# Performance work log

Hardware: AMD Instinct MI355X
Metric: run time of the kernel (lower is better)

The kernel has to match this reference:

```python
import jax, jax.numpy as jnp
import numpy as np

B, SEQ, VOCAB, DIM, DEPTH, HEADS, DH, M, FF, LABELS = 4, 2048, 4096, 768, 6, 12, 64, 256, 3072, 2
INNER = HEADS * DH
EPS_K = 1e-4  # FAVOR+ kernel eps
EPS_LN = 1e-5


def setup_inputs() -> dict:
    key = jax.random.key(0)
    ks = jax.random.split(key, 16)
    g = lambda k, shape: (jax.random.normal(k, shape, jnp.float32) * 0.02)
    return {
        "x": jax.random.randint(ks[0], (B, SEQ), 0, VOCAB),
        "token_emb": g(ks[1], (VOCAB, DIM)),
        "pos_emb": g(ks[2], (SEQ, DIM)),
        "ln1_g": jnp.ones((DEPTH, DIM)), "ln1_b": jnp.zeros((DEPTH, DIM)),
        "Wq": g(ks[3], (DEPTH, DIM, INNER)),
        "Wk": g(ks[4], (DEPTH, DIM, INNER)),
        "Wv": g(ks[5], (DEPTH, DIM, INNER)),
        "Wo": g(ks[6], (DEPTH, INNER, DIM)), "bo": jnp.zeros((DEPTH, DIM)),
        "proj": jax.random.normal(ks[7], (DEPTH, M, DH), jnp.float32),  # FAVOR+ random projections (buffer)
        "ln2_g": jnp.ones((DEPTH, DIM)), "ln2_b": jnp.zeros((DEPTH, DIM)),
        "W1": g(ks[8], (DEPTH, DIM, FF)), "b1": jnp.zeros((DEPTH, FF)),
        "W2": g(ks[9], (DEPTH, FF, DIM)), "b2": jnp.zeros((DEPTH, DIM)),
        "lnf_g": jnp.ones((DIM,)), "lnf_b": jnp.zeros((DIM,)),
        "Wp": g(ks[10], (DIM, DIM)), "bp": jnp.zeros((DIM,)),
        "Wc": g(ks[11], (DIM, LABELS)), "bc": jnp.zeros((LABELS,)),
    }


def layernorm(x, g, b):
    mu = jnp.mean(x, -1, keepdims=True)
    var = jnp.mean(jnp.square(x - mu), -1, keepdims=True)
    return (x - mu) * jax.lax.rsqrt(var + EPS_LN) * g + b


def softmax_kernel(x, proj, is_query):
    # x: [b,h,n,d]  proj: [m,d]   (FAVOR+ positive softmax features)
    d = x.shape[-1]
    m = proj.shape[0]
    dn = d ** -0.25            # data normalizer 1/sqrt(sqrt(d))
    ratio = m ** -0.5
    xd = jnp.einsum('bhnd,md->bhnm', x * dn, proj)
    diag = 0.5 * jnp.sum(jnp.square(x), -1, keepdims=True) * (dn * dn)  # [b,h,n,1]
    if is_query:
        stab = jnp.max(xd, axis=-1, keepdims=True)
    else:
        stab = jnp.max(xd, axis=(-2, -1), keepdims=True)
    return ratio * (jnp.exp(xd - diag - stab) + EPS_K)


def favor_attention(y, Wq, Wk, Wv, Wo, bo, proj):
    b, n, _ = y.shape
    split = lambda t: t.reshape(b, n, HEADS, DH).transpose(0, 2, 1, 3)  # -> bhnd
    q, k, v = split(y @ Wq), split(y @ Wk), split(y @ Wv)
    qp = softmax_kernel(q, proj, True)    # [b,h,n,m]
    kp = softmax_kernel(k, proj, False)   # [b,h,n,m]
    k_sum = jnp.sum(kp, axis=2)                                  # [b,h,m]
    d_inv = 1.0 / jnp.einsum('bhnm,bhm->bhn', qp, k_sum)
    ctx = jnp.einsum('bhnm,bhnd->bhmd', kp, v)                   # [b,h,m,d]
    out = jnp.einsum('bhmd,bhnm,bhn->bhnd', ctx, qp, d_inv)
    out = out.transpose(0, 2, 1, 3).reshape(b, n, INNER)
    return out @ Wo + bo


def reference(x, token_emb, pos_emb, ln1_g, ln1_b, Wq, Wk, Wv, Wo, bo, proj,
              ln2_g, ln2_b, W1, b1, W2, b2, lnf_g, lnf_b, Wp, bp, Wc, bc):
    n = x.shape[1]
    h = token_emb[x] + pos_emb[None, :n]
    for l in range(DEPTH):
        h = h + favor_attention(layernorm(h, ln1_g[l], ln1_b[l]),
                                Wq[l], Wk[l], Wv[l], Wo[l], bo[l], proj[l])
        y = layernorm(h, ln2_g[l], ln2_b[l])
        h = h + (jax.nn.gelu(y @ W1[l] + b1[l], approximate=False) @ W2[l] + b2[l])
    h = layernorm(h, lnf_g, lnf_b)
    pooled = jnp.tanh(h[:, 0] @ Wp + bp)   # BertPooler on first token
    return pooled @ Wc + bc                 # [B, LABELS]
```

## Files before the change

### kernel.cpp

```cpp
#include <hip/hip_runtime.h>
#include <hip/hip_bf16.h>
#include <math.h>

#define B_ 4
#define SEQ_ 2048
#define DIM_ 768
#define DEPTH_ 6
#define HEADS_ 12
#define DH_ 64
#define MF_ 256
#define FF_ 3072
#define ROWS_ 8192
#define BH_ 48
#define QKVW_ 2304
#define DN_ 0.3535533905932738f
#define RATIO_ 0.0625f
#define EPSK_ 1e-4f
#define EPSLN_ 1e-5f

typedef unsigned short u16;
typedef unsigned int   u32;
typedef __bf16 bf16x8 __attribute__((ext_vector_type(8)));
typedef u16    u16x8  __attribute__((ext_vector_type(8)));
typedef float  f32x4  __attribute__((ext_vector_type(4)));

__device__ inline u16 f2bf(float x){
  u32 u = __builtin_bit_cast(u32, x);
  return (u16)((u + 0x7FFFu + ((u>>16)&1u)) >> 16);
}
__device__ inline float bf2f(u16 v){ return __builtin_bit_cast(float, (u32)v<<16); }

__device__ inline void gload16(const u16* g, u16* lds){
  __builtin_amdgcn_global_load_lds(
    (const __attribute__((address_space(1))) u32*)(const void*)g,
    (__attribute__((address_space(3))) u32*)(void*)lds, 16, 0, 0);
}

__global__ void embed_kernel(const int* __restrict__ x, const float4* __restrict__ tok,
                             const float4* __restrict__ pos, float4* __restrict__ h){
  const int C4 = DIM_/4;
  long total = (long)ROWS_*C4;
  for (long i = (long)blockIdx.x*blockDim.x + threadIdx.x; i < total;
       i += (long)gridDim.x*blockDim.x){
    int row = (int)(i / C4); int c = (int)(i - (long)row*C4);
    int n = row & (SEQ_-1);
    float4 a = tok[(long)x[row]*C4 + c];
    float4 p = pos[(long)n*C4 + c];
    float4 o; o.x=a.x+p.x; o.y=a.y+p.y; o.z=a.z+p.z; o.w=a.w+p.w;
    h[i] = o;
  }
}

__global__ __launch_bounds__(256) void ln_kernel(const float* __restrict__ X,
                          const float* __restrict__ g, const float* __restrict__ bta,
                          u16* __restrict__ Y){
  int row = blockIdx.x; int t = threadIdx.x;
  const float* xr = X + (long)row*DIM_;
  float v0 = xr[t], v1 = xr[t+256], v2 = xr[t+512];
  float s = v0+v1+v2;
  float ss = v0*v0+v1*v1+v2*v2;
  int lane = t&63, wid = t>>6;
  #pragma unroll
  for (int off=32; off; off>>=1){ s += __shfl_xor(s,off); ss += __shfl_xor(ss,off); }
  __shared__ float red[8];
  if (lane==0){ red[wid]=s; red[4+wid]=ss; }
  __syncthreads();
  s  = red[0]+red[1]+red[2]+red[3];
  ss = red[4]+red[5]+red[6]+red[7];
  float mu  = s*(1.0f/DIM_);
  float var = ss*(1.0f/DIM_) - mu*mu;
  float rs  = rsqrtf(var + EPSLN_);
  u16* yr = Y + (long)row*DIM_;
  yr[t]     = f2bf((v0-mu)*rs*g[t]     + bta[t]);
  yr[t+256] = f2bf((v1-mu)*rs*g[t+256] + bta[t+256]);
  yr[t+512] = f2bf((v2-mu)*rs*g[t+512] + bta[t+512]);
}

__global__ __launch_bounds__(256) void tconv_kernel(const float* __restrict__ W,
        u16* __restrict__ WT, int K, int N){
  __shared__ float tile[32][33];
  int n0 = blockIdx.x*32, k0 = blockIdx.y*32;
  int tx = threadIdx.x & 31, ty = threadIdx.x >> 5;
  #pragma unroll
  for (int i=0;i<32;i+=8) tile[ty+i][tx] = W[(long)(k0+ty+i)*N + n0+tx];
  __syncthreads();
  #pragma unroll
  for (int i=0;i<32;i+=8) WT[(long)(n0+ty+i)*K + k0+tx] = f2bf(tile[tx][ty+i]);
}

__global__ __launch_bounds__(256) void tconv4_kernel(const float* __restrict__ Wq,
        const float* __restrict__ Wk, const float* __restrict__ Wv,
        const float* __restrict__ Wo, u16* __restrict__ dst){
  __shared__ float tile[32][33];
  int z = blockIdx.z;
  const float* W = (z==0)?Wq:(z==1)?Wk:(z==2)?Wv:Wo;
  u16* WT = dst + (long)z*589824;
  int n0 = blockIdx.x*32, k0 = blockIdx.y*32;
  int tx = threadIdx.x & 31, ty = threadIdx.x >> 5;
  #pragma unroll
  for (int i=0;i<32;i+=8) tile[ty+i][tx] = W[(long)(k0+ty+i)*768 + n0+tx];
  __syncthreads();
  #pragma unroll
  for (int i=0;i<32;i+=8) WT[(long)(n0+ty+i)*768 + k0+tx] = f2bf(tile[tx][ty+i]);
}

template<int FM, int FN, int WM, int WN, int ACT, int CMODE, int BATCH>
__global__ __launch_bounds__(256) void mgemm(const u16* __restrict__ A,
     const u16* __restrict__ BT, const float* __restrict__ bias,
     void* __restrict__ Cv, const float* __restrict__ scale,
     int M, int N, int K, int ldC){
  (void)M;
  constexpr int BM = WM*FM*16, BN = WN*FN*16;
  constexpr int ACH = BM/16, BCH = BN/16;
  __shared__ u16 As[BM*64];
  __shared__ u16 Bs[BN*64];
  int tid = threadIdx.x; int w = tid>>6, l = tid&63;
  int bx, by;
  if (BATCH){ bx = blockIdx.x; by = blockIdx.y; }
  else {
    int bid = blockIdx.y*gridDim.x + blockIdx.x;
    int cpx = (gridDim.x*gridDim.y) >> 3;
    int swz = (bid & 7)*cpx + (bid >> 3);
    bx = swz % gridDim.x; by = swz / gridDim.x;
  }
  int m0 = by*BM, n0 = bx*BN;
  long coff = 0, srow0 = 0;
  if (BATCH){
    int z = blockIdx.z;
    A  += (long)z*2048*K;
    BT += (long)z*(long)N*K;
    coff  = (long)(z/HEADS_)*SEQ_*(long)ldC + (long)(z%HEADS_)*64;
    srow0 = (long)z*SEQ_;
  }
  f32x4 acc[FM][FN];
  #pragma unroll
  for (int i=0;i<FM;i++)
    #pragma unroll
    for (int j=0;j<FN;j++) acc[i][j] = (f32x4){0.f,0.f,0.f,0.f};

  const int row_l = l>>2, cq_l = l&3;
  const int wm = w / WN, wn = w % WN;
  const int kq = l>>4, rl15 = l&15;

  for (int k0=0; k0<K; k0+=64){
    __syncthreads();
    for (int c = w; c < 2*ACH; c += 4){
      int rc = c>>1, ks = c&1;
      int r = rc*16 + row_l;
      int gq = cq_l ^ ((r>>1)&3);
      gload16(A + (long)(m0+r)*K + k0 + ks*32 + gq*8, As + c*512);
    }
    for (int c = w; c < 2*BCH; c += 4){
      int rc = c>>1, ks = c&1;
      int r = rc*16 + row_l;
      int gq = cq_l ^ ((r>>1)&3);
      gload16(BT + (long)(n0+r)*K + k0 + ks*32 + gq*8, Bs + c*512);
    }
    __syncthreads();
    #pragma unroll
    for (int ks=0; ks<2; ks++){
      bf16x8 af[FM], bfr[FN];
      #pragma unroll
      for (int mi=0; mi<FM; mi++){
        int rr = (wm*FM + mi)*16 + rl15;
        int g = kq ^ ((rr>>1)&3);
        af[mi] = *(const bf16x8*)(As + ((rr>>4)*2 + ks)*512 + (rr&15)*32 + g*8);
      }
      #pragma unroll
      for (int ni=0; ni<FN; ni++){
        int rr = (wn*FN + ni)*16 + rl15;
        int g = kq ^ ((rr>>1)&3);
        bfr[ni] = *(const bf16x8*)(Bs + ((rr>>4)*2 + ks)*512 + (rr&15)*32 + g*8);
      }
      #pragma unroll
      for (int mi=0; mi<FM; mi++)
        #pragma unroll
        for (int ni=0; ni<FN; ni++)
          acc[mi][ni] = __builtin_amdgcn_mfma_f32_16x16x32_bf16(af[mi], bfr[ni], acc[mi][ni], 0, 0, 0);
    }
  }

  int cc = l&15, rq = l>>4;
  #pragma unroll
  for (int mi=0; mi<FM; mi++){
    #pragma unroll
    for (int ni=0; ni<FN; ni++){
      int gcol = n0 + (wn*FN+ni)*16 + cc;
      float bv = bias ? bias[gcol] : 0.f;
      #pragma unroll
      for (int r4=0; r4<4; r4++){
        int grow = m0 + (wm*FM+mi)*16 + rq*4 + r4;
        float v = acc[mi][ni][r4] + bv;
        if (ACT) v = 0.5f*v*(1.0f + erff(v*0.70710678118654752f));
        if (CMODE==1){
          float* C = (float*)Cv;
          C[(long)grow*ldC + gcol] += v;
        } else if (CMODE==2){
          v *= scale[srow0 + grow];
          ((u16*)Cv)[coff + (long)grow*ldC + gcol] = f2bf(v);
        } else {
          ((u16*)Cv)[(long)grow*ldC + gcol] = f2bf(v);
        }
      }
    }
  }
}

__global__ void projcvt_kernel(const float* __restrict__ p, u16* __restrict__ hi,
                               u16* __restrict__ lo){
  int i = blockIdx.x*256 + threadIdx.x;
  float v = p[i];
  u16 h = f2bf(v);
  hi[i] = h;
  lo[i] = f2bf(v - bf2f(h));
}

__global__ __launch_bounds__(256) void diag2_kernel(const u16* __restrict__ qkvp,
        float* __restrict__ diagq, float* __restrict__ diagk){
  int chunk = blockIdx.x, z = blockIdx.y, which = blockIdx.z, t = threadIdx.x;
  const u16* X = qkvp + (which ? 768 : 0);
  float* outp = which ? diagk : diagq;
  int n = chunk*256 + t;
  const u16* r = X + ((long)(z/HEADS_)*SEQ_ + n)*QKVW_ + (z%HEADS_)*DH_;
  float s = 0.f;
  #pragma unroll
  for (int q=0;q<8;q++){
    u16x8 v = *(const u16x8*)(r + q*8);
    #pragma unroll
    for (int j=0;j<8;j++){ float f = bf2f(v[j]); s += f*f; }
  }
  outp[(long)z*SEQ_ + n] = 0.5f*DN_*DN_*s;
}

template<int MODE>
__global__ __launch_bounds__(256) void featgemm(const u16* __restrict__ X,
     const u16* __restrict__ PB, const float* __restrict__ diag,
     const float* __restrict__ stab, u16* __restrict__ kp,
     float* __restrict__ fmaxp){
  __shared__ u16 As[128*32];
  __shared__ u16 Bs[128*32];
  __shared__ float wred[4];
  int tid = threadIdx.x; int w = tid>>6, l = tid&63;
  int n0 = blockIdx.x*128, m0 = blockIdx.y*128;
  int z = blockIdx.z;
  const u16* A = X + (long)(z/HEADS_)*SEQ_*QKVW_ + (z%HEADS_)*DH_;
  f32x4 acc[4][4];
  #pragma unroll
  for (int i=0;i<4;i++)
    #pragma unroll
    for (int j=0;j<4;j++) acc[i][j] = (f32x4){0.f,0.f,0.f,0.f};
  const int row_l = l>>2, cq_l = l&3;
  const int wm = w>>1, wn = w&1;
  const int kq = l>>4, rl15 = l&15;

  for (int k0=0; k0<64; k0+=32){
    __syncthreads();
    for (int c = w; c < 8; c += 4){
      int r = c*16 + row_l;
      int gq = cq_l ^ ((r>>1)&3);
      gload16(A + (long)(m0+r)*QKVW_ + k0 + gq*8, As + c*512);
    }
    for (int c = w; c < 8; c += 4){
      int r = c*16 + row_l;
      int gq = cq_l ^ ((r>>1)&3);
      gload16(PB + (long)(n0+r)*64 + k0 + gq*8, Bs + c*512);
    }
    __syncthreads();
    bf16x8 af[4], bfr[4];
    #pragma unroll
    for (int mi=0; mi<4; mi++){
      int rr = (wm*4 + mi)*16 + rl15;
      int g = kq ^ ((rr>>1)&3);
      af[mi] = *(const bf16x8*)(As + rr*32 + g*8);
    }
    #pragma unroll
    for (int ni=0; ni<4; ni++){
      int rr = (wn*4 + ni)*16 + rl15;
      int g = kq ^ ((rr>>1)&3);
      bfr[ni] = *(const bf16x8*)(Bs + rr*32 + g*8);
    }
    #pragma unroll
    for (int mi=0; mi<4; mi++)
      #pragma unroll
      for (int ni=0; ni<4; ni++)
        acc[mi][ni] = __builtin_amdgcn_mfma_f32_16x16x32_bf16(af[mi], bfr[ni], acc[mi][ni], 0, 0, 0);
  }

  if (MODE==0){
    float bm = -1e30f;
    #pragma unroll
    for (int mi=0;mi<4;mi++)
      #pragma unroll
      for (int ni=0;ni<4;ni++)
        #pragma unroll
        for (int r4=0;r4<4;r4++) bm = fmaxf(bm, acc[mi][ni][r4]);
    bm *= DN_;
    #pragma unroll
    for (int off=32; off; off>>=1) bm = fmaxf(bm, __shfl_xor(bm,off));
    if (l==0) wred[w] = bm;
    __syncthreads();
    if (tid==0)
      fmaxp[z*32 + blockIdx.y*2 + blockIdx.x] =
        fmaxf(fmaxf(wred[0],wred[1]),fmaxf(wred[2],wred[3]));
  } else {
    __shared__ float ksred[128][8];
    float st = stab[z];
    int cc = l&15, rq = l>>4;
    #pragma unroll
    for (int ni=0; ni<4; ni++){
      int gcol = n0 + (wn*4+ni)*16 + cc;
      float cs = 0.f;
      #pragma unroll
      for (int mi=0; mi<4; mi++){
        #pragma unroll
        for (int r4=0; r4<4; r4++){
          int grow = m0 + (wm*4+mi)*16 + rq*4 + r4;
          float v = acc[mi][ni][r4]*DN_;
          float e = RATIO_*(expf(v - diag[(long)z*SEQ_ + grow] - st) + EPSK_);
          u16 eb = f2bf(e);
          kp[((long)z*SEQ_ + grow)*MF_ + gcol] = eb;
          cs += bf2f(eb);
        }
      }
      ksred[(wn*4+ni)*16 + cc][wm*4 + rq] = cs;
    }
    __syncthreads();
    if (tid < 128){
      float s = 0.f;
      #pragma unroll
      for (int q=0;q<8;q++) s += ksred[tid][q];
      fmaxp[((long)z*16 + blockIdx.y)*MF_ + n0 + tid] = s;
    }
  }
}

__global__ void fmax_reduce(const float* __restrict__ fmaxp, float* __restrict__ stab){
  int z = blockIdx.x, t = threadIdx.x;
  float m = (t<32) ? fmaxp[z*32+t] : -1e30f;
  #pragma unroll
  for (int off=32; off; off>>=1) m = fmaxf(m, __shfl_xor(m,off));
  if (t==0) stab[z] = m;
}

__global__ void ksum_reduce(const float* __restrict__ part, float* __restrict__ ksum){
  int z = blockIdx.x; int t = threadIdx.x;
  float s = 0.f;
  #pragma unroll
  for (int c=0;c<16;c++) s += part[((long)z*16+c)*MF_ + t];
  ksum[z*MF_+t] = s;
}

__global__ __launch_bounds__(256) void qfeatgemm(const u16* __restrict__ X,
     const u16* __restrict__ PH, const u16* __restrict__ PL,
     const float* __restrict__ diagq, const float* __restrict__ ksum,
     u16* __restrict__ qp, float* __restrict__ dinv){
  __shared__ u16 As[64*32];
  __shared__ u16 Bh[256*32];
  __shared__ u16 Bl[256*32];
  __shared__ float ksl[256];
  __shared__ float rmax[64][4];
  __shared__ float rsum[64][4];
  int tid = threadIdx.x; int w = tid>>6, l = tid&63;
  int n0 = blockIdx.x*64;
  int z = blockIdx.y;
  const u16* A = X + (long)(z/HEADS_)*SEQ_*QKVW_ + (z%HEADS_)*DH_;
  ksl[tid] = ksum[(long)z*MF_ + tid];
  f32x4 acc[4][4];
  #pragma unroll
  for (int i=0;i<4;i++)
    #pragma unroll
    for (int j=0;j<4;j++) acc[i][j] = (f32x4){0.f,0.f,0.f,0.f};
  const int row_l = l>>2, cq_l = l&3;
  const int kq = l>>4, rl15 = l&15;

  for (int k0=0; k0<64; k0+=32){
    __syncthreads();
    {
      int r = w*16 + row_l;
      int gq = cq_l ^ ((r>>1)&3);
      gload16(A + (long)(n0+r)*QKVW_ + k0 + gq*8, As + w*512);
    }
    for (int c = w; c < 16; c += 4){
      int r = c*16 + row_l;
      int gq = cq_l ^ ((r>>1)&3);
      gload16(PH + (long)r*64 + k0 + gq*8, Bh + c*512);
      gload16(PL + (long)r*64 + k0 + gq*8, Bl + c*512);
    }
    __syncthreads();
    bf16x8 af[4], bh[4], bl[4];
    #pragma unroll
    for (int mi=0; mi<4; mi++){
      int rr = mi*16 + rl15;
      int g = kq ^ ((rr>>1)&3);
      af[mi] = *(const bf16x8*)(As + rr*32 + g*8);
    }
    #pragma unroll
    for (int ni=0; ni<4; ni++){
      int rr = (w*4 + ni)*16 + rl15;
      int g = kq ^ ((rr>>1)&3);
      bh[ni] = *(const bf16x8*)(Bh + rr*32 + g*8);
      bl[ni] = *(const bf16x8*)(Bl + rr*32 + g*8);
    }
    #pragma unroll
    for (int mi=0; mi<4; mi++)
      #pragma unroll
      for (int ni=0; ni<4; ni++){
        acc[mi][ni] = __builtin_amdgcn_mfma_f32_16x16x32_bf16(af[mi], bh[ni], acc[mi][ni], 0, 0, 0);
        acc[mi][ni] = __builtin_amdgcn_mfma_f32_16x16x32_bf16(af[mi], bl[ni], acc[mi][ni], 0, 0, 0);
      }
  }

  int cc = l&15, rq = l>>4;
  #pragma unroll
  for (int mi=0; mi<4; mi++){
    #pragma unroll
    for (int r4=0; r4<4; r4++){
      float pm = fmaxf(fmaxf(acc[mi][0][r4],acc[mi][1][r4]),
                       fmaxf(acc[mi][2][r4],acc[mi][3][r4]));
      pm = fmaxf(pm, __shfl_xor(pm,1)); pm = fmaxf(pm, __shfl_xor(pm,2));
      pm = fmaxf(pm, __shfl_xor(pm,4)); pm = fmaxf(pm, __shfl_xor(pm,8));
      if (cc==0) rmax[mi*16 + rq*4 + r4][w] = pm;
    }
  }
  __syncthreads();
  #pragma unroll
  for (int mi=0; mi<4; mi++){
    #pragma unroll
    for (int r4=0; r4<4; r4++){
      int row = mi*16 + rq*4 + r4;
      float mx = fmaxf(fmaxf(rmax[row][0],rmax[row][1]),
                       fmaxf(rmax[row][2],rmax[row][3])) * DN_;
      float dq = diagq[(long)z*SEQ_ + n0 + row];
      float dv = 0.f;
      #pragma unroll
      for (int ni=0; ni<4; ni++){
        int col = w*64 + ni*16 + cc;
        float qpv = RATIO_*(expf(acc[mi][ni][r4]*DN_ - dq - mx) + EPSK_);
        u16 qb = f2bf(qpv);
        qp[((long)z*SEQ_ + n0 + row)*MF_ + col] = qb;
        dv += bf2f(qb)*ksl[col];
      }
      dv += __shfl_xor(dv,1); dv += __shfl_xor(dv,2);
      dv += __shfl_xor(dv,4); dv += __shfl_xor(dv,8);
      if (cc==0) rsum[row][w] = dv;
    }
  }
  __syncthreads();
  if (tid < 64){
    float s = rsum[tid][0]+rsum[tid][1]+rsum[tid][2]+rsum[tid][3];
    dinv[(long)z*SEQ_ + n0 + tid] = 1.0f/s;
  }
}

__global__ __launch_bounds__(256) void ctxgemm(const u16* __restrict__ qkv,
     const u16* __restrict__ kp, float* __restrict__ part){
  int kc = blockIdx.x;
  int z  = blockIdx.y;
  int b = z/HEADS_, hh = z%HEADS_;
  int tid = threadIdx.x; int w = tid>>6, l = tid&63;
  __shared__ u16 Vt[64*40];
  __shared__ u16 Kpt[256*40];
  f32x4 acc[4][4];
  #pragma unroll
  for (int i=0;i<4;i++)
    #pragma unroll
    for (int j=0;j<4;j++) acc[i][j] = (f32x4){0.f,0.f,0.f,0.f};
  int n_l = tid&31, grp = tid>>5;
  const int kq = l>>4, rl15 = l&15;
  const long vbase = (long)b*SEQ_*QKVW_ + hh*DH_ + 1536;
  const long kbase = (long)z*SEQ_*MF_;

  for (int s=0; s<32; s++){
    int nG = kc*1024 + s*32 + n_l;
    __syncthreads();
    {
      u16x8 v = *(const u16x8*)(qkv + vbase + (long)nG*QKVW_ + grp*8);
      #pragma unroll
      for (int j=0;j<8;j++) Vt[(grp*8+j)*40 + n_l] = v[j];
    }
    {
      const u16* src = kp + kbase + (long)nG*MF_ + grp*32;
      #pragma unroll
      for (int q=0;q<4;q++){
        u16x8 v = *(const u16x8*)(src + q*8);
        #pragma unroll
        for (int j=0;j<8;j++) Kpt[(grp*32+q*8+j)*40 + n_l] = v[j];
      }
    }
    __syncthreads();
    bf16x8 af[4], bfr[4];
    #pragma unroll
    for (int mi=0; mi<4; mi++)
      af[mi] = *(const bf16x8*)(Vt + (mi*16+rl15)*40 + kq*8);
    #pragma unroll
    for (int ni=0; ni<4; ni++)
      bfr[ni] = *(const bf16x8*)(Kpt + ((w*4+ni)*16+rl15)*40 + kq*8);
    #pragma unroll
    for (int mi=0; mi<4; mi++)
      #pragma unroll
      for (int ni=0; ni<4; ni++)
        acc[mi][ni] = __builtin_amdgcn_mfma_f32_16x16x32_bf16(af[mi], bfr[ni], acc[mi][ni], 0, 0, 0);
  }

  int cc = l&15, rq = l>>4;
  float* pb = part + ((long)kc*BH_ + z)*(64*MF_);
  #pragma unroll
  for (int mi=0; mi<4; mi++){
    #pragma unroll
    for (int ni=0; ni<4; ni++){
      int m = (w*4+ni)*16 + cc;
      #pragma unroll
      for (int r4=0; r4<4; r4++){
        int d = mi*16 + rq*4 + r4;
        pb[(long)d*MF_ + m] = acc[mi][ni][r4];
      }
    }
  }
}

__global__ void ctx_reduce2(const float* __restrict__ part, u16* __restrict__ ctxT){
  const long NT = (long)BH_*64*MF_;
  for (long i = (long)blockIdx.x*256 + threadIdx.x; i < NT; i += (long)gridDim.x*256){
    ctxT[i] = f2bf(part[i] + part[NT + i]);
  }
}

__global__ __launch_bounds__(256) void lnrow0_kernel(const float* __restrict__ h,
                          const float* __restrict__ g, const float* __restrict__ bta,
                          float* __restrict__ xnf){
  int b = blockIdx.x; int t = threadIdx.x;
  const float* row = h + (long)b*SEQ_*DIM_;
  float v0=row[t], v1=row[t+256], v2=row[t+512];
  float s = v0+v1+v2, ss = v0*v0+v1*v1+v2*v2;
  int lane=t&63, wid=t>>6;
  #pragma unroll
  for (int off=32; off; off>>=1){ s += __shfl_xor(s,off); ss += __shfl_xor(ss,off); }
  __shared__ float red[8];
  if (lane==0){ red[wid]=s; red[4+wid]=ss; }
  __syncthreads();
  s  = red[0]+red[1]+red[2]+red[3];
  ss = red[4]+red[5]+red[6]+red[7];
  float mu = s*(1.0f/DIM_);
  float var = ss*(1.0f/DIM_) - mu*mu;
  float rs = rsqrtf(var + EPSLN_);
  float* xr = xnf + b*DIM_;
  xr[t]     = (v0-mu)*rs*g[t]     + bta[t];
  xr[t+256] = (v1-mu)*rs*g[t+256] + bta[t+256];
  xr[t+512] = (v2-mu)*rs*g[t+512] + bta[t+512];
}

__global__ __launch_bounds__(256) void poolmv_kernel(const float* __restrict__ xnf,
        const float* __restrict__ Wp, const float* __restrict__ bp,
        float* __restrict__ pooled){
  int c = blockIdx.x;
  int b = blockIdx.y;
  __shared__ float xs[768];
  __shared__ float red[64][5];
  int t = threadIdx.x;
  xs[t] = xnf[b*DIM_+t]; xs[t+256] = xnf[b*DIM_+t+256]; xs[t+512] = xnf[b*DIM_+t+512];
  __syncthreads();
  int col_l = t & 63, seg = t >> 6;
  int col = c*64 + col_l;
  const float* wp = Wp + col;
  float a = 0.f;
  #pragma unroll 4
  for (int i = seg*192; i < (seg+1)*192; i++) a += xs[i]*wp[(long)i*DIM_];
  red[col_l][seg] = a;
  __syncthreads();
  if (t < 64){
    float s = red[t][0]+red[t][1]+red[t][2]+red[t][3] + bp[c*64+t];
    pooled[b*DIM_ + c*64 + t] = tanhf(s);
  }
}

__global__ __launch_bounds__(256) void cls_kernel(const float* __restrict__ pooled,
        const float* __restrict__ Wc, const float* __restrict__ bc,
        float* __restrict__ out){
  int t = threadIdx.x;
  int b = t >> 6, lane = t & 63;
  float a0 = 0.f, a1 = 0.f;
  for (int i = lane; i < 768; i += 64){
    float p = pooled[b*DIM_ + i];
    a0 += p*Wc[i*2]; a1 += p*Wc[i*2+1];
  }
  #pragma unroll
  for (int off=32; off; off>>=1){ a0 += __shfl_xor(a0,off); a1 += __shfl_xor(a1,off); }
  if (lane==0){ out[b*2] = a0 + bc[0]; out[b*2+1] = a1 + bc[1]; }
}

extern "C" void kernel_launch(void* const* d_in, const int* in_sizes, int n_in,
                              void* d_out, int out_size, void* d_ws, size_t ws_size,
                              hipStream_t stream) {
  (void)in_sizes; (void)n_in; (void)out_size; (void)ws_size;
  const int*   x    = (const int*)  d_in[0];
  const float* tok  = (const float*)d_in[1];
  const float* pos  = (const float*)d_in[2];
  const float* ln1g = (const float*)d_in[3];
  const float* ln1b = (const float*)d_in[4];
  const float* Wq   = (const float*)d_in[5];
  const float* Wk   = (const float*)d_in[6];
  const float* Wv   = (const float*)d_in[7];
  const float* Wo   = (const float*)d_in[8];
  const float* bo   = (const float*)d_in[9];
  const float* proj = (const float*)d_in[10];
  const float* ln2g = (const float*)d_in[11];
  const float* ln2b = (const float*)d_in[12];
  const float* W1   = (const float*)d_in[13];
  const float* b1   = (const float*)d_in[14];
  const float* W2   = (const float*)d_in[15];
  const float* b2   = (const float*)d_in[16];
  const float* lnfg = (const float*)d_in[17];
  const float* lnfb = (const float*)d_in[18];
  const float* Wp   = (const float*)d_in[19];
  const float* bp   = (const float*)d_in[20];
  const float* Wc   = (const float*)d_in[21];
  const float* bc   = (const float*)d_in[22];
  float* out = (float*)d_out;

  char* wsb = (char*)d_ws;
  float* h     = (float*)(wsb + 0);
  u16*   ybf   = (u16*)  (wsb + 25165824);
  float* ctxp2 = (float*)(wsb + 25165824);
  float* diag  = (float*)(wsb + 31457280);
  float* diagq = (float*)(wsb + 31850496);
  float* ksp   = (float*)(wsb + 32243712);
  float* fmaxp = (float*)(wsb + 33030144);
  u16*   projbf= (u16*)  (wsb + 33036288);
  u16*   projlo= (u16*)  (wsb + 33069056);
  float* stab  = (float*)(wsb + 33101824);
  float* xnf   = (float*)(wsb + 25165824);
  float* pooled= (float*)(wsb + 25178112);
  u16*   qkv   = (u16*)  (wsb + 37748736);
  u16*   ffnbf = (u16*)  (wsb + 75497472);
  u16*   kp    = (u16*)  (wsb + 75497472);
  u16*   qp    = (u16*)  (wsb + 75497472);
  u16*   wT    = (u16*)  (wsb + 125829120);
  u16*   ctxT  = (u16*)  (wsb + 139984896);
  float* ksum  = (float*)(wsb + 141557760);
  float* dinv  = (float*)(wsb + 141606912);
  u16* attnbf  = ybf;

  u16* wtq = wT;
  u16* wto = wT + 1769472;
  u16* wt1 = wT + 2359296;
  u16* wt2 = wT + 4718592;

  embed_kernel<<<2048,256,0,stream>>>(x,(const float4*)tok,(const float4*)pos,(float4*)h);

  dim3 gD64(6, 128);
  dim3 gQKV(18, 64);
  dim3 gF(24, 64);
  dim3 gQ2(1, 16, BH_);
  dim3 gFG(2, 16, BH_);
  dim3 gQF(32, BH_);

  for (int l=0; l<DEPTH_; l++){
    const float* wq  = Wq + (size_t)l*DIM_*DIM_;
    const float* wk  = Wk + (size_t)l*DIM_*DIM_;
    const float* wv  = Wv + (size_t)l*DIM_*DIM_;
    const float* wo  = Wo + (size_t)l*DIM_*DIM_;
    const float* prj = proj + (size_t)l*MF_*DH_;
    const float* w1  = W1 + (size_t)l*DIM_*FF_;
    const float* w2  = W2 + (size_t)l*FF_*DIM_;

    tconv4_kernel<<<dim3(24,24,4),256,0,stream>>>(wq, wk, wv, wo, wtq);
    tconv_kernel<<<dim3(96,24),256,0,stream>>>(w1, wt1, 768, 3072);
    tconv_kernel<<<dim3(24,96),256,0,stream>>>(w2, wt2, 3072, 768);

    ln_kernel<<<ROWS_,256,0,stream>>>(h, ln1g+(size_t)l*DIM_, ln1b+(size_t)l*DIM_, ybf);
    mgemm<4,4,2,2,0,0,0><<<gQKV,256,0,stream>>>(ybf, wtq, nullptr, qkv, nullptr, ROWS_, QKVW_, 768, QKVW_);

    projcvt_kernel<<<64,256,0,stream>>>(prj, projbf, projlo);
    diag2_kernel<<<dim3(8,BH_,2),256,0,stream>>>(qkv, diagq, diag);
    featgemm<0><<<gFG,256,0,stream>>>(qkv + 768, projbf, nullptr, nullptr, nullptr, fmaxp);
    fmax_reduce<<<BH_,64,0,stream>>>(fmaxp, stab);
    featgemm<1><<<gFG,256,0,stream>>>(qkv + 768, projbf, diag, stab, kp, ksp);
    ctxgemm<<<dim3(2,BH_),256,0,stream>>>(qkv, kp, ctxp2);
    ctx_reduce2<<<768,256,0,stream>>>(ctxp2, ctxT);
    ksum_reduce<<<BH_,256,0,stream>>>(ksp, ksum);

    qfeatgemm<<<gQF,256,0,stream>>>(qkv, projbf, projlo, diagq, ksum, qp, dinv);
    mgemm<2,4,4,1,0,2,1><<<gQ2,256,0,stream>>>(qp, ctxT, nullptr, attnbf, dinv, SEQ_, 64, 256, 768);

    mgemm<2,4,2,2,0,1,0><<<gD64,256,0,stream>>>(attnbf, wto, bo+(size_t)l*DIM_, h, nullptr, ROWS_, 768, 768, 768);

    ln_kernel<<<ROWS_,256,0,stream>>>(h, ln2g+(size_t)l*DIM_, ln2b+(size_t)l*DIM_, ybf);
    mgemm<4,4,2,2,1,0,0><<<gF,256,0,stream>>>(ybf, wt1, b1+(size_t)l*FF_, ffnbf, nullptr, ROWS_, 3072, 768, 3072);
    mgemm<2,4,2,2,0,1,0><<<gD64,256,0,stream>>>(ffnbf, wt2, b2+(size_t)l*DIM_, h, nullptr, ROWS_, 768, 3072, 768);
  }

  lnrow0_kernel<<<B_,256,0,stream>>>(h, lnfg, lnfb, xnf);
  poolmv_kernel<<<dim3(12,B_),256,0,stream>>>(xnf, Wp, bp, pooled);
  cls_kernel<<<1,256,0,stream>>>(pooled, Wc, bc, out);
}
```

Measured before the change: 2.256 ms.

## Fuse small attention helper kernels into featgemm, qfeatgemm, ctxgemm and transposes

Removes several small launches per layer. Projection conversion moves into the weight-transpose kernel, and the two FF transposes merge into one launch. The diag computation moves into featgemm/qfeatgemm using the shared-memory tiles, and the fmax and ksum reductions are done in the consuming kernels. ctxgemm now runs one block per head over the full sequence, writing bf16 directly and dropping the split-K partials and reduce kernel. This cuts launch overhead and intermediate traffic, but ctxgemm now gets only 48 blocks, which lowers parallelism.

```diff
diff --git a/kernel.cpp b/kernel.cpp
--- a/kernel.cpp
+++ b/kernel.cpp
@@ -76,23 +76,27 @@
   yr[t+512] = f2bf((v2-mu)*rs*g[t+512] + bta[t+512]);
 }
 
-__global__ __launch_bounds__(256) void tconv_kernel(const float* __restrict__ W,
-        u16* __restrict__ WT, int K, int N){
+__global__ __launch_bounds__(256) void tconv5_kernel(const float* __restrict__ Wq,
+        const float* __restrict__ Wk, const float* __restrict__ Wv,
+        const float* __restrict__ Wo, const float* __restrict__ prj,
+        u16* __restrict__ dst, u16* __restrict__ phi, u16* __restrict__ plo){
+  int z = blockIdx.z;
+  if (z == 4){
+    int bid = blockIdx.y*24 + blockIdx.x;
+    if (bid < 16){
+      int i = bid*1024 + threadIdx.x*4;
+      float4 v = *(const float4*)(prj + i);
+      float vv[4] = {v.x, v.y, v.z, v.w};
+      #pragma unroll
+      for (int j=0;j<4;j++){
+        u16 hh = f2bf(vv[j]);
+        phi[i+j] = hh;
+        plo[i+j] = f2bf(vv[j] - bf2f(hh));
+      }
+    }
+    return;
+  }
   __shared__ float tile[32][33];
-  int n0 = blockIdx.x*32, k0 = blockIdx.y*32;
-  int tx = threadIdx.x & 31, ty = threadIdx.x >> 5;
-  #pragma unroll
-  for (int i=0;i<32;i+=8) tile[ty+i][tx] = W[(long)(k0+ty+i)*N + n0+tx];
-  __syncthreads();
-  #pragma unroll
-  for (int i=0;i<32;i+=8) WT[(long)(n0+ty+i)*K + k0+tx] = f2bf(tile[tx][ty+i]);
-}
-
-__global__ __launch_bounds__(256) void tconv4_kernel(const float* __restrict__ Wq,
-        const float* __restrict__ Wk, const float* __restrict__ Wv,
-        const float* __restrict__ Wo, u16* __restrict__ dst){
-  __shared__ float tile[32][33];
-  int z = blockIdx.z;
   const float* W = (z==0)?Wq:(z==1)?Wk:(z==2)?Wv:Wo;
   u16* WT = dst + (long)z*589824;
   int n0 = blockIdx.x*32, k0 = blockIdx.y*32;
@@ -102,6 +106,21 @@
   __syncthreads();
   #pragma unroll
   for (int i=0;i<32;i+=8) WT[(long)(n0+ty+i)*768 + k0+tx] = f2bf(tile[tx][ty+i]);
+}
+
+__global__ __launch_bounds__(256) void tconvFF_kernel(const float* __restrict__ W1,
+        const float* __restrict__ W2, u16* __restrict__ wt1, u16* __restrict__ wt2){
+  __shared__ float tile[32][33];
+  int z = blockIdx.z;
+  const float* W; u16* WT; int K, N, n0, k0;
+  if (z==0){ W=W1; WT=wt1; K=768;  N=3072; n0=blockIdx.x*32; k0=blockIdx.y*32; }
+  else     { W=W2; WT=wt2; K=3072; N=768;  n0=blockIdx.y*32; k0=blockIdx.x*32; }
+  int tx = threadIdx.x & 31, ty = threadIdx.x >> 5;
+  #pragma unroll
+  for (int i=0;i<32;i+=8) tile[ty+i][tx] = W[(long)(k0+ty+i)*N + n0+tx];
+  __syncthreads();
+  #pragma unroll
+  for (int i=0;i<32;i+=8) WT[(long)(n0+ty+i)*K + k0+tx] = f2bf(tile[tx][ty+i]);
 }
 
 template<int FM, int FN, int WM, int WN, int ACT, int CMODE, int BATCH>
@@ -206,49 +225,31 @@
   }
 }
 
-__global__ void projcvt_kernel(const float* __restrict__ p, u16* __restrict__ hi,
-                               u16* __restrict__ lo){
-  int i = blockIdx.x*256 + threadIdx.x;
-  float v = p[i];
-  u16 h = f2bf(v);
-  hi[i] = h;
-  lo[i] = f2bf(v - bf2f(h));
-}
-
-__global__ __launch_bounds__(256) void diag2_kernel(const u16* __restrict__ qkvp,
-        float* __restrict__ diagq, float* __restrict__ diagk){
-  int chunk = blockIdx.x, z = blockIdx.y, which = blockIdx.z, t = threadIdx.x;
-  const u16* X = qkvp + (which ? 768 : 0);
-  float* outp = which ? diagk : diagq;
-  int n = chunk*256 + t;
-  const u16* r = X + ((long)(z/HEADS_)*SEQ_ + n)*QKVW_ + (z%HEADS_)*DH_;
-  float s = 0.f;
-  #pragma unroll
-  for (int q=0;q<8;q++){
-    u16x8 v = *(const u16x8*)(r + q*8);
-    #pragma unroll
-    for (int j=0;j<8;j++){ float f = bf2f(v[j]); s += f*f; }
-  }
-  outp[(long)z*SEQ_ + n] = 0.5f*DN_*DN_*s;
-}
-
 template<int MODE>
 __global__ __launch_bounds__(256) void featgemm(const u16* __restrict__ X,
-     const u16* __restrict__ PB, const float* __restrict__ diag,
-     const float* __restrict__ stab, u16* __restrict__ kp,
-     float* __restrict__ fmaxp){
+     const u16* __restrict__ PB, u16* __restrict__ kp,
+     float* __restrict__ fmaxbuf, float* __restrict__ ksp){
   __shared__ u16 As[128*32];
   __shared__ u16 Bs[128*32];
   __shared__ float wred[4];
+  __shared__ float diag_s[128];
   int tid = threadIdx.x; int w = tid>>6, l = tid&63;
   int n0 = blockIdx.x*128, m0 = blockIdx.y*128;
   int z = blockIdx.z;
   const u16* A = X + (long)(z/HEADS_)*SEQ_*QKVW_ + (z%HEADS_)*DH_;
+  float st = 0.f;
+  if (MODE==1){
+    float mm = (l<32) ? fmaxbuf[z*32 + l] : -1e30f;
+    #pragma unroll
+    for (int off=32; off; off>>=1) mm = fmaxf(mm, __shfl_xor(mm,off));
+    st = mm;
+  }
   f32x4 acc[4][4];
   #pragma unroll
   for (int i=0;i<4;i++)
     #pragma unroll
     for (int j=0;j<4;j++) acc[i][j] = (f32x4){0.f,0.f,0.f,0.f};
+  float rdiag = 0.f;
   const int row_l = l>>2, cq_l = l&3;
   const int wm = w>>1, wn = w&1;
   const int kq = l>>4, rl15 = l&15;
@@ -266,6 +267,20 @@
       gload16(PB + (long)(n0+r)*64 + k0 + gq*8, Bs + c*512);
     }
     __syncthreads();
+    if (MODE==1){
+      int dr = tid>>1, dc = tid&1;
+      const u16* rb = As + (dr>>4)*512 + (dr&15)*32 + dc*16;
+      u16x8 a0 = *(const u16x8*)rb;
+      u16x8 a1 = *(const u16x8*)(rb + 8);
+      float s = 0.f;
+      #pragma unroll
+      for (int j=0;j<8;j++){
+        float f0 = bf2f(a0[j]), f1 = bf2f(a1[j]);
+        s += f0*f0 + f1*f1;
+      }
+      s += __shfl_xor(s,1);
+      rdiag += s;
+    }
     bf16x8 af[4], bfr[4];
     #pragma unroll
     for (int mi=0; mi<4; mi++){
@@ -300,11 +315,12 @@
     if (l==0) wred[w] = bm;
     __syncthreads();
     if (tid==0)
-      fmaxp[z*32 + blockIdx.y*2 + blockIdx.x] =
+      fmaxbuf[z*32 + blockIdx.y*2 + blockIdx.x] =
         fmaxf(fmaxf(wred[0],wred[1]),fmaxf(wred[2],wred[3]));
   } else {
+    if ((tid&1)==0) diag_s[tid>>1] = 0.5f*DN_*DN_*rdiag;
+    __syncthreads();
     __shared__ float ksred[128][8];
-    float st = stab[z];
     int cc = l&15, rq = l>>4;
     #pragma unroll
     for (int ni=0; ni<4; ni++){
@@ -314,11 +330,11 @@
       for (int mi=0; mi<4; mi++){
         #pragma unroll
         for (int r4=0; r4<4; r4++){
-          int grow = m0 + (wm*4+mi)*16 + rq*4 + r4;
+          int lrow = (wm*4+mi)*16 + rq*4 + r4;
           float v = acc[mi][ni][r4]*DN_;
-          float e = RATIO_*(expf(v - diag[(long)z*SEQ_ + grow] - st) + EPSK_);
+          float e = RATIO_*(expf(v - diag_s[lrow] - st) + EPSK_);
           u16 eb = f2bf(e);
-          kp[((long)z*SEQ_ + grow)*MF_ + gcol] = eb;
+          kp[((long)z*SEQ_ + m0 + lrow)*MF_ + gcol] = eb;
           cs += bf2f(eb);
         }
       }
@@ -329,47 +345,37 @@
       float s = 0.f;
       #pragma unroll
       for (int q=0;q<8;q++) s += ksred[tid][q];
-      fmaxp[((long)z*16 + blockIdx.y)*MF_ + n0 + tid] = s;
-    }
-  }
-}
-
-__global__ void fmax_reduce(const float* __restrict__ fmaxp, float* __restrict__ stab){
-  int z = blockIdx.x, t = threadIdx.x;
-  float m = (t<32) ? fmaxp[z*32+t] : -1e30f;
-  #pragma unroll
-  for (int off=32; off; off>>=1) m = fmaxf(m, __shfl_xor(m,off));
-  if (t==0) stab[z] = m;
-}
-
-__global__ void ksum_reduce(const float* __restrict__ part, float* __restrict__ ksum){
-  int z = blockIdx.x; int t = threadIdx.x;
-  float s = 0.f;
-  #pragma unroll
-  for (int c=0;c<16;c++) s += part[((long)z*16+c)*MF_ + t];
-  ksum[z*MF_+t] = s;
+      ksp[((long)z*16 + blockIdx.y)*MF_ + n0 + tid] = s;
+    }
+  }
 }
 
 __global__ __launch_bounds__(256) void qfeatgemm(const u16* __restrict__ X,
      const u16* __restrict__ PH, const u16* __restrict__ PL,
-     const float* __restrict__ diagq, const float* __restrict__ ksum,
-     u16* __restrict__ qp, float* __restrict__ dinv){
+     const float* __restrict__ ksp, u16* __restrict__ qp, float* __restrict__ dinv){
   __shared__ u16 As[64*32];
   __shared__ u16 Bh[256*32];
   __shared__ u16 Bl[256*32];
   __shared__ float ksl[256];
+  __shared__ float dqs[64];
   __shared__ float rmax[64][4];
   __shared__ float rsum[64][4];
   int tid = threadIdx.x; int w = tid>>6, l = tid&63;
   int n0 = blockIdx.x*64;
   int z = blockIdx.y;
   const u16* A = X + (long)(z/HEADS_)*SEQ_*QKVW_ + (z%HEADS_)*DH_;
-  ksl[tid] = ksum[(long)z*MF_ + tid];
+  {
+    float s = 0.f;
+    #pragma unroll
+    for (int c=0;c<16;c++) s += ksp[((long)z*16+c)*MF_ + tid];
+    ksl[tid] = s;
+  }
   f32x4 acc[4][4];
   #pragma unroll
   for (int i=0;i<4;i++)
     #pragma unroll
     for (int j=0;j<4;j++) acc[i][j] = (f32x4){0.f,0.f,0.f,0.f};
+  float rdiag = 0.f;
   const int row_l = l>>2, cq_l = l&3;
   const int kq = l>>4, rl15 = l&15;
 
@@ -387,6 +393,16 @@
       gload16(PL + (long)r*64 + k0 + gq*8, Bl + c*512);
     }
     __syncthreads();
+    {
+      int dr = tid>>2, dq4 = tid&3;
+      const u16* rb = As + (dr>>4)*512 + (dr&15)*32 + dq4*8;
+      u16x8 a0 = *(const u16x8*)rb;
+      float s = 0.f;
+      #pragma unroll
+      for (int j=0;j<8;j++){ float f = bf2f(a0[j]); s += f*f; }
+      s += __shfl_xor(s,1); s += __shfl_xor(s,2);
+      rdiag += s;
+    }
     bf16x8 af[4], bh[4], bl[4];
     #pragma unroll
     for (int mi=0; mi<4; mi++){
@@ -409,6 +425,9 @@
         acc[mi][ni] = __builtin_amdgcn_mfma_f32_16x16x32_bf16(af[mi], bl[ni], acc[mi][ni], 0, 0, 0);
       }
   }
+
+  if ((tid&3)==0) dqs[tid>>2] = 0.5f*DN_*DN_*rdiag;
+  __syncthreads();
 
   int cc = l&15, rq = l>>4;
   #pragma unroll
@@ -430,7 +449,7 @@
       int row = mi*16 + rq*4 + r4;
       float mx = fmaxf(fmaxf(rmax[row][0],rmax[row][1]),
                        fmaxf(rmax[row][2],rmax[row][3])) * DN_;
-      float dq = diagq[(long)z*SEQ_ + n0 + row];
+      float dq = dqs[row];
       float dv = 0.f;
       #pragma unroll
       for (int ni=0; ni<4; ni++){
@@ -453,9 +472,8 @@
 }
 
 __global__ __launch_bounds__(256) void ctxgemm(const u16* __restrict__ qkv,
-     const u16* __restrict__ kp, float* __restrict__ part){
-  int kc = blockIdx.x;
-  int z  = blockIdx.y;
+     const u16* __restrict__ kp, u16* __restrict__ ctxT){
+  int z  = blockIdx.x;
   int b = z/HEADS_, hh = z%HEADS_;
   int tid = threadIdx.x; int w = tid>>6, l = tid&63;
   __shared__ u16 Vt[64*40];
@@ -470,8 +488,8 @@
   const long vbase = (long)b*SEQ_*QKVW_ + hh*DH_ + 1536;
   const long kbase = (long)z*SEQ_*MF_;
 
-  for (int s=0; s<32; s++){
-    int nG = kc*1024 + s*32 + n_l;
+  for (int s=0; s<64; s++){
+    int nG = s*32 + n_l;
     __syncthreads();
     {
       u16x8 v = *(const u16x8*)(qkv + vbase + (long)nG*QKVW_ + grp*8);
@@ -503,7 +521,7 @@
   }
 
   int cc = l&15, rq = l>>4;
-  float* pb = part + ((long)kc*BH_ + z)*(64*MF_);
+  u16* cb = ctxT + (long)z*(64*MF_);
   #pragma unroll
   for (int mi=0; mi<4; mi++){
     #pragma unroll
@@ -512,52 +530,38 @@
       #pragma unroll
       for (int r4=0; r4<4; r4++){
         int d = mi*16 + rq*4 + r4;
-        pb[(long)d*MF_ + m] = acc[mi][ni][r4];
-      }
-    }
-  }
-}
-
-__global__ void ctx_reduce2(const float* __restrict__ part, u16* __restrict__ ctxT){
-  const long NT = (long)BH_*64*MF_;
-  for (long i = (long)blockIdx.x*256 + threadIdx.x; i < NT; i += (long)gridDim.x*256){
-    ctxT[i] = f2bf(part[i] + part[NT + i]);
-  }
-}
-
-__global__ __launch_bounds__(256) void lnrow0_kernel(const float* __restrict__ h,
-                          const float* __restrict__ g, const float* __restrict__ bta,
-                          float* __restrict__ xnf){
-  int b = blockIdx.x; int t = threadIdx.x;
-  const float* row = h + (long)b*SEQ_*DIM_;
-  float v0=row[t], v1=row[t+256], v2=row[t+512];
-  float s = v0+v1+v2, ss = v0*v0+v1*v1+v2*v2;
-  int lane=t&63, wid=t>>6;
-  #pragma unroll
-  for (int off=32; off; off>>=1){ s += __shfl_xor(s,off); ss += __shfl_xor(ss,off); }
-  __shared__ float red[8];
-  if (lane==0){ red[wid]=s; red[4+wid]=ss; }
-  __syncthreads();
-  s  = red[0]+red[1]+red[2]+red[3];
-  ss = red[4]+red[5]+red[6]+red[7];
-  float mu = s*(1.0f/DIM_);
-  float var = ss*(1.0f/DIM_) - mu*mu;
-  float rs = rsqrtf(var + EPSLN_);
-  float* xr = xnf + b*DIM_;
-  xr[t]     = (v0-mu)*rs*g[t]     + bta[t];
-  xr[t+256] = (v1-mu)*rs*g[t+256] + bta[t+256];
-  xr[t+512] = (v2-mu)*rs*g[t+512] + bta[t+512];
-}
-
-__global__ __launch_bounds__(256) void poolmv_kernel(const float* __restrict__ xnf,
+        cb[(long)d*MF_ + m] = f2bf(acc[mi][ni][r4]);
+      }
+    }
+  }
+}
+
+__global__ __launch_bounds__(256) void poolmv_kernel(const float* __restrict__ h,
+        const float* __restrict__ g, const float* __restrict__ bta,
         const float* __restrict__ Wp, const float* __restrict__ bp,
         float* __restrict__ pooled){
   int c = blockIdx.x;
   int b = blockIdx.y;
   __shared__ float xs[768];
+  __shared__ float red8[8];
   __shared__ float red[64][5];
   int t = threadIdx.x;
-  xs[t] = xnf[b*DIM_+t]; xs[t+256] = xnf[b*DIM_+t+256]; xs[t+512] = xnf[b*DIM_+t+512];
+  const float* row = h + (long)b*SEQ_*DIM_;
+  float v0=row[t], v1=row[t+256], v2=row[t+512];
+  float s = v0+v1+v2, ss = v0*v0+v1*v1+v2*v2;
+  int lane=t&63, wid=t>>6;
+  #pragma unroll
+  for (int off=32; off; off>>=1){ s += __shfl_xor(s,off); ss += __shfl_xor(ss,off); }
+  if (lane==0){ red8[wid]=s; red8[4+wid]=ss; }
+  __syncthreads();
+  s  = red8[0]+red8[1]+red8[2]+red8[3];
+  ss = red8[4]+red8[5]+red8[6]+red8[7];
+  float mu = s*(1.0f/DIM_);
+  float var = ss*(1.0f/DIM_) - mu*mu;
+  float rs = rsqrtf(var + EPSLN_);
+  xs[t]     = (v0-mu)*rs*g[t]     + bta[t];
+  xs[t+256] = (v1-mu)*rs*g[t+256] + bta[t+256];
+  xs[t+512] = (v2-mu)*rs*g[t+512] + bta[t+512];
   __syncthreads();
   int col_l = t & 63, seg = t >> 6;
   int col = c*64 + col_l;
@@ -568,8 +572,8 @@
   red[col_l][seg] = a;
   __syncthreads();
   if (t < 64){
-    float s = red[t][0]+red[t][1]+red[t][2]+red[t][3] + bp[c*64+t];
-    pooled[b*DIM_ + c*64 + t] = tanhf(s);
+    float sv = red[t][0]+red[t][1]+red[t][2]+red[t][3] + bp[c*64+t];
+    pooled[b*DIM_ + c*64 + t] = tanhf(sv);
   }
 }
 
@@ -620,15 +624,8 @@
   char* wsb = (char*)d_ws;
   float* h     = (float*)(wsb + 0);
   u16*   ybf   = (u16*)  (wsb + 25165824);
-  float* ctxp2 = (float*)(wsb + 25165824);
-  float* diag  = (float*)(wsb + 31457280);
-  float* diagq = (float*)(wsb + 31850496);
   float* ksp   = (float*)(wsb + 32243712);
   float* fmaxp = (float*)(wsb + 33030144);
-  u16*   projbf= (u16*)  (wsb + 33036288);
-  u16*   projlo= (u16*)  (wsb + 33069056);
-  float* stab  = (float*)(wsb + 33101824);
-  float* xnf   = (float*)(wsb + 25165824);
   float* pooled= (float*)(wsb + 25178112);
   u16*   qkv   = (u16*)  (wsb + 37748736);
   u16*   ffnbf = (u16*)  (wsb + 75497472);
@@ -636,8 +633,9 @@
   u16*   qp    = (u16*)  (wsb + 75497472);
   u16*   wT    = (u16*)  (wsb + 125829120);
   u16*   ctxT  = (u16*)  (wsb + 139984896);
-  float* ksum  = (float*)(wsb + 141557760);
-  float* dinv  = (float*)(wsb + 141606912);
+  float* dinv  = (float*)(wsb + 141557760);
+  u16*   projbf= (u16*)  (wsb + 141950976);
+  u16*   projlo= (u16*)  (wsb + 141983744);
   u16* attnbf  = ybf;
 
   u16* wtq = wT;
@@ -663,23 +661,17 @@
     const float* w1  = W1 + (size_t)l*DIM_*FF_;
     const float* w2  = W2 + (size_t)l*FF_*DIM_;
 
-    tconv4_kernel<<<dim3(24,24,4),256,0,stream>>>(wq, wk, wv, wo, wtq);
-    tconv_kernel<<<dim3(96,24),256,0,stream>>>(w1, wt1, 768, 3072);
-    tconv_kernel<<<dim3(24,96),256,0,stream>>>(w2, wt2, 3072, 768);
+    tconv5_kernel<<<dim3(24,24,5),256,0,stream>>>(wq, wk, wv, wo, prj, wtq, projbf, projlo);
+    tconvFF_kernel<<<dim3(96,24,2),256,0,stream>>>(w1, w2, wt1, wt2);
 
     ln_kernel<<<ROWS_,256,0,stream>>>(h, ln1g+(size_t)l*DIM_, ln1b+(size_t)l*DIM_, ybf);
     mgemm<4,4,2,2,0,0,0><<<gQKV,256,0,stream>>>(ybf, wtq, nullptr, qkv, nullptr, ROWS_, QKVW_, 768, QKVW_);
 
-    projcvt_kernel<<<64,256,0,stream>>>(prj, projbf, projlo);
-    diag2_kernel<<<dim3(8,BH_,2),256,0,stream>>>(qkv, diagq, diag);
-    featgemm<0><<<gFG,256,0,stream>>>(qkv + 768, projbf, nullptr, nullptr, nullptr, fmaxp);
-    fmax_reduce<<<BH_,64,0,stream>>>(fmaxp, stab);
-    featgemm<1><<<gFG,256,0,stream>>>(qkv + 768, projbf, diag, stab, kp, ksp);
-    ctxgemm<<<dim3(2,BH_),256,0,stream>>>(qkv, kp, ctxp2);
-    ctx_reduce2<<<768,256,0,stream>>>(ctxp2, ctxT);
-    ksum_reduce<<<BH_,256,0,stream>>>(ksp, ksum);
-
-    qfeatgemm<<<gQF,256,0,stream>>>(qkv, projbf, projlo, diagq, ksum, qp, dinv);
+    featgemm<0><<<gFG,256,0,stream>>>(qkv + 768, projbf, nullptr, fmaxp, nullptr);
+    featgemm<1><<<gFG,256,0,stream>>>(qkv + 768, projbf, kp, fmaxp, ksp);
+    ctxgemm<<<BH_,256,0,stream>>>(qkv, kp, ctxT);
+
+    qfeatgemm<<<gQF,256,0,stream>>>(qkv, projbf, projlo, ksp, qp, dinv);
     mgemm<2,4,4,1,0,2,1><<<gQ2,256,0,stream>>>(qp, ctxT, nullptr, attnbf, dinv, SEQ_, 64, 256, 768);
 
     mgemm<2,4,2,2,0,1,0><<<gD64,256,0,stream>>>(attnbf, wto, bo+(size_t)l*DIM_, h, nullptr, ROWS_, 768, 768, 768);
@@ -689,7 +681,6 @@
     mgemm<2,4,2,2,0,1,0><<<gD64,256,0,stream>>>(ffnbf, wt2, b2+(size_t)l*DIM_, h, nullptr, ROWS_, 768, 3072, 768);
   }
 
-  lnrow0_kernel<<<B_,256,0,stream>>>(h, lnfg, lnfb, xnf);
-  poolmv_kernel<<<dim3(12,B_),256,0,stream>>>(xnf, Wp, bp, pooled);
+  poolmv_kernel<<<dim3(12,B_),256,0,stream>>>(h, lnfg, lnfb, Wp, bp, pooled);
   cls_kernel<<<1,256,0,stream>>>(pooled, Wc, bc, out);
 }
```

Measured after the change: 2.406 ms. 1.07x slower.
